# Performance work log

Hardware: AMD Instinct MI355X
Metric: run time of the kernel (lower is better)

The kernel has to match this reference:

```python
import jax, jax.numpy as jnp
import numpy as np
from jax import lax

B = 128
IM = 56  # im_size: 56 -> 48 -> 20 -> 6 spatial, 256*6*6/8 = 1152 primary capsules


def _conv(x, w, b, stride):
    y = lax.conv_general_dilated(x, w, (stride, stride), 'VALID',
                                 dimension_numbers=('NCHW', 'OIHW', 'NCHW'))
    return y + b[None, :, None, None]


def _squash(t, eps=1e-8):
    sn = jnp.sum(t * t, axis=-1, keepdims=True)
    return (sn / (1.0 + sn)) * t / jnp.sqrt(sn + eps)


def setup_inputs() -> dict:
    key = jax.random.key(0)
    ks = jax.random.split(key, 9)
    s = 0.02
    f32 = jnp.float32
    return {
        'x': jax.random.normal(ks[0], (B, 1, IM, IM), f32),
        'conv1_w': jax.random.normal(ks[1], (256, 1, 9, 9), f32) * s,
        'conv1_b': jnp.zeros((256,), f32),
        'conv2_w': jax.random.normal(ks[2], (256, 256, 9, 9), f32) * s,
        'conv2_b': jnp.zeros((256,), f32),
        'prim_w': jax.random.normal(ks[3], (256, 256, 9, 9), f32) * s,
        'prim_b': jnp.zeros((256,), f32),
        'W_digit': jax.random.normal(ks[4], (10, 1152, 8, 16), f32) * s,  # Linear(9216,16) per digit, reshaped
        'b_digit': jnp.zeros((10, 16), f32),
        'rec_w1': jax.random.normal(ks[5], (160, 512), f32) * s,
        'rec_b1': jnp.zeros((512,), f32),
        'rec_w2': jax.random.normal(ks[6], (512, 1024), f32) * s,
        'rec_b2': jnp.zeros((1024,), f32),
        'rec_w3': jax.random.normal(ks[7], (1024, IM * IM), f32) * s,
        'rec_b3': jnp.zeros((IM * IM,), f32),
    }


def reference(x, conv1_w, conv1_b, conv2_w, conv2_b, prim_w, prim_b,
              W_digit, b_digit, rec_w1, rec_b1, rec_w2, rec_b2, rec_w3, rec_b3):
    out = jax.nn.relu(_conv(x, conv1_w, conv1_b, 1))    # [B,256,48,48]
    out = jax.nn.relu(_conv(out, conv2_w, conv2_b, 2))  # [B,256,20,20]
    out = jax.nn.relu(_conv(out, prim_w, prim_b, 2))    # [B,256,6,6]
    u = _squash(out.reshape(out.shape[0], -1, 8))       # [B,1152,8]
    # fused 10-way digit-capsule transform: u_hat[b,i,j,:] = W[j,i] @ u[b,i]
    u_hat = jnp.einsum('bid,jido->bijo', u, W_digit)    # [B,1152,10,16]
    b_ij = jnp.zeros(u_hat.shape[:3], u_hat.dtype)      # [B,1152,10]
    num_iterations = 3
    v = None
    for it in range(num_iterations):
        c = jax.nn.softmax(b_ij, axis=1)                       # coupling over input capsules
        s_j = jnp.einsum('bij,bijo->bjo', c, u_hat) + b_digit  # [B,10,16]
        v = _squash(s_j)
        if it < num_iterations - 1:
            b_ij = b_ij + jnp.einsum('bijo,bjo->bij', u_hat, v)
    rec = v.reshape(v.shape[0], -1)                     # [B,160]
    rec = jax.nn.relu(rec @ rec_w1 + rec_b1)
    rec = jax.nn.relu(rec @ rec_w2 + rec_b2)
    rec = jax.nn.sigmoid(rec @ rec_w3 + rec_b3)         # [B,3136]
    return (v, rec)
```

## Files before the change

kernel.cpp:

```cpp
#include <hip/hip_runtime.h>
#include <hip/hip_bf16.h>

typedef float f32x4 __attribute__((ext_vector_type(4)));
typedef __bf16 bf16x8 __attribute__((ext_vector_type(8)));
typedef __bf16 bf16x4 __attribute__((ext_vector_type(4)));

#define AS1 __attribute__((address_space(1)))
#define AS3 __attribute__((address_space(3)))

__device__ __forceinline__ void gload16(const void* g, void* l) {
    __builtin_amdgcn_global_load_lds((AS1 unsigned int*)g, (AS3 unsigned int*)l, 16, 0, 0);
}

__device__ __forceinline__ float bfu(unsigned short u) {
    return __uint_as_float((unsigned)u << 16);
}

__global__ __launch_bounds__(256) void prep_w_kernel(const float* __restrict__ wA,
                                                     const float* __restrict__ wB,
                                                     __hip_bfloat16* __restrict__ wpA,
                                                     __hip_bfloat16* __restrict__ wpB,
                                                     const float* __restrict__ c1w,
                                                     __hip_bfloat16* __restrict__ wb,
                                                     const float* __restrict__ x,
                                                     __hip_bfloat16* __restrict__ xb) {
    int bid = blockIdx.x;
    int t = threadIdx.x;
    if (bid == 1024) {
        float tmp[81];
#pragma unroll
        for (int k = 0; k < 81; ++k) tmp[k] = c1w[t * 81 + k];
#pragma unroll
        for (int ks = 0; ks < 9; ++ks)
#pragma unroll
            for (int e = 0; e < 8; ++e)
                wb[(ks * 256 + t) * 8 + e] = __float2bfloat16(tmp[ks * 9 + e]);
#pragma unroll
        for (int e = 0; e < 8; ++e)
            wb[(9 * 256 + t) * 8 + e] = __float2bfloat16(tmp[e * 9 + 8]);
        wb[(10 * 256 + t) * 8 + 0] = __float2bfloat16(tmp[80]);
#pragma unroll
        for (int e = 1; e < 8; ++e) wb[(10 * 256 + t) * 8 + e] = __float2bfloat16(0.f);
#pragma unroll
        for (int e = 0; e < 8; ++e) wb[(11 * 256 + t) * 8 + e] = __float2bfloat16(0.f);
        return;
    }
    if (bid >= 1025) {
        long i4 = (long)(bid - 1025) * 1024 + t * 4;
        float4 v = *(const float4*)(x + i4);
        bf16x4 o = {(__bf16)v.x, (__bf16)v.y, (__bf16)v.z, (__bf16)v.w};
        *(bf16x4*)((__bf16*)xb + i4) = o;
        return;
    }
    __shared__ float wl[4 * 32 * 81];
    const float* w = (bid < 512) ? wA : wB;
    __hip_bfloat16* wp = (bid < 512) ? wpA : wpB;
    bid &= 511;
    int icg = bid & 7;
    int oc4 = (bid >> 3) & 31;
    int nblk = bid >> 8;
    int ocg0 = nblk * 128 + oc4 * 4;
    int ic0 = icg * 32;
    for (int f = t; f < 4 * 2592; f += 256) {
        int o = f / 2592;
        int rest = f - o * 2592;
        wl[f] = w[(ocg0 + o) * 20736 + ic0 * 81 + rest];
    }
    __syncthreads();
    for (int idx = t; idx < 81 * 128; idx += 256) {
        int kyx = idx >> 7;
        int o = (idx >> 5) & 3;
        int i = idx & 31;
        long dst = (long)(((kyx * 8 + icg) * 2 + nblk) * 128 + (oc4 * 4 + o)) * 32 + i;
        wp[dst] = __float2bfloat16(wl[o * 2592 + i * 81 + kyx]);
    }
}

__global__ __launch_bounds__(256) void conv1_mfma_kernel(const __hip_bfloat16* __restrict__ xb,
                                                         const __hip_bfloat16* __restrict__ wb,
                                                         const float* __restrict__ bias,
                                                         __hip_bfloat16* __restrict__ out) {
    __shared__ __bf16 Asl[640];
    int bid = blockIdx.x;
    int b = bid / 24, mb2 = bid - b * 24;
    int oy0 = mb2 * 2;
    int t = threadIdx.x;
    int lane = t & 63, wc = t >> 6;
    int q = lane >> 4;

    const __bf16* src = (const __bf16*)xb + b * 3136 + oy0 * 56;
    for (int idx = t; idx < 640; idx += 256) {
        int iy = idx >> 6, col = idx & 63;
        Asl[idx] = (col < 56) ? src[iy * 56 + col] : (__bf16)0.f;
    }

    bf16x8 Bf[3][4];
#pragma unroll
    for (int s = 0; s < 3; ++s)
#pragma unroll
        for (int ni = 0; ni < 4; ++ni) {
            int col = wc * 64 + ni * 16 + (lane & 15);
            Bf[s][ni] = *(const bf16x8*)(wb + ((s * 4 + q) * 256 + col) * 8);
        }

    f32x4 acc[6][4];
#pragma unroll
    for (int i = 0; i < 6; ++i)
#pragma unroll
        for (int j = 0; j < 4; ++j) acc[i][j] = (f32x4){0.f, 0.f, 0.f, 0.f};

    __syncthreads();

#pragma unroll
    for (int s = 0; s < 3; ++s) {
        int ks = s * 4 + q;
        bf16x8 af[6];
#pragma unroll
        for (int mi = 0; mi < 6; ++mi) {
            int r = mi * 16 + (lane & 15);
            int oyl = (r >= 48) ? 1 : 0;
            int ox = r - 48 * oyl;
            bf16x8 v;
            if (ks < 9) {
                __builtin_memcpy(&v, &Asl[(oyl + ks) * 64 + ox], 16);
            } else if (ks == 9) {
#pragma unroll
                for (int e = 0; e < 8; ++e) v[e] = Asl[(oyl + e) * 64 + ox + 8];
            } else if (ks == 10) {
#pragma unroll
                for (int e = 0; e < 8; ++e) v[e] = (__bf16)0.f;
                v[0] = Asl[(oyl + 8) * 64 + ox + 8];
            } else {
#pragma unroll
                for (int e = 0; e < 8; ++e) v[e] = (__bf16)0.f;
            }
            af[mi] = v;
        }
#pragma unroll
        for (int mi = 0; mi < 6; ++mi)
#pragma unroll
            for (int ni = 0; ni < 4; ++ni)
                acc[mi][ni] = __builtin_amdgcn_mfma_f32_16x16x32_bf16(af[mi], Bf[s][ni], acc[mi][ni], 0, 0, 0);
    }

    long m0 = (long)b * 2304 + mb2 * 96;
#pragma unroll
    for (int mi = 0; mi < 6; ++mi)
#pragma unroll
        for (int ni = 0; ni < 4; ++ni) {
            int col = wc * 64 + ni * 16 + (lane & 15);
            float bs = bias[col];
#pragma unroll
            for (int r2 = 0; r2 < 4; ++r2) {
                int row = mi * 16 + q * 4 + r2;
                float vv = acc[mi][ni][r2] + bs;
                vv = vv > 0.f ? vv : 0.f;
                out[(m0 + row) * 256 + col] = __float2bfloat16(vv);
            }
        }
}

__global__ __launch_bounds__(512, 2) void conv2_img_kernel(const __hip_bfloat16* __restrict__ in,
                                                           const __hip_bfloat16* __restrict__ wp,
                                                           const float* __restrict__ bias,
                                                           __hip_bfloat16* __restrict__ out) {
    __shared__ __hip_bfloat16 Ald[75264];
    int bid = blockIdx.x;
    int wg = (bid & 7) * 32 + (bid >> 3);
    int b = wg >> 1, nblk = wg & 1;
    int t = threadIdx.x;
    int lane = t & 63, wid = t >> 6;
    int wr = wid >> 1, wc = wid & 1;
    int ch8 = lane >> 4;

    const __hip_bfloat16* imgbase = in + (long)b * (48 * 48 * 256);
    const __hip_bfloat16* wpn = wp + (long)nblk * 4096 + (wc * 64 + (lane & 15)) * 32 + ch8 * 8;

    int qbase[7];
#pragma unroll
    for (int mi = 0; mi < 7; ++mi) {
        int ml = wr * 96 + mi * 16 + (lane & 15);
        int oy = ml / 20, ox = ml - oy * 20;
        qbase[mi] = ((2 * oy) * 49 + 2 * ox) * 4 + ch8;
    }

    f32x4 acc[7][4];
#pragma unroll
    for (int i = 0; i < 7; ++i)
#pragma unroll
        for (int j = 0; j < 4; ++j) acc[i][j] = (f32x4){0.f, 0.f, 0.f, 0.f};

    auto stageA = [&](int icg) {
#pragma unroll
        for (int c = 0; c < 3; ++c) {
            uint4 v[6];
#pragma unroll
            for (int j = 0; j < 6; ++j) {
                int gi = t + (c * 6 + j) * 512;
                int lrow = gi >> 2;
                int iy = lrow / 48;
                int col = lrow - iy * 48;
                if (iy > 46) iy = 46;
                v[j] = *(const uint4*)(imgbase + (iy * 48 + col) * 256 + icg * 32 + (gi & 3) * 8);
            }
#pragma unroll
            for (int j = 0; j < 6; ++j) {
                int gi = t + (c * 6 + j) * 512;
                int lrow = gi >> 2;
                int iy = lrow / 48;
                int col = lrow - iy * 48;
                int dst = (iy * 49 + col) * 4 + (gi & 3);
                int phys = dst ^ ((dst >> 3) & 7);
                *(uint4*)((char*)Ald + phys * 16) = v[j];
            }
        }
    };

    bf16x8 af_e[7], af_o[7], Be[4], Bo[4];
    int pf_kdelta = 0, pf_kx = 0, pf_ky = 0;
    auto prefA = [&](bf16x8* af) {
#pragma unroll
        for (int mi = 0; mi < 7; ++mi) {
            int qg = qbase[mi] + pf_kdelta;
            int phys = qg ^ ((qg >> 3) & 7);
            af[mi] = *(const bf16x8*)((const char*)Ald + phys * 16);
        }
        ++pf_kx; pf_kdelta += 4;
        if (pf_kx == 9) { pf_kx = 0; ++pf_ky; pf_kdelta = pf_ky * 196; }
    };
    auto domfma = [&](bf16x8* af, bf16x8* bf) {
        __builtin_amdgcn_s_setprio(1);
#pragma unroll
        for (int mi = 0; mi < 7; ++mi)
#pragma unroll
            for (int ni = 0; ni < 4; ++ni)
                acc[mi][ni] = __builtin_amdgcn_mfma_f32_16x16x32_bf16(af[mi], bf[ni], acc[mi][ni], 0, 0, 0);
        __builtin_amdgcn_s_setprio(0);
    };

    for (int icg = 0; icg < 8; ++icg) {
        const __hip_bfloat16* wpi = wpn + (long)icg * 8192;
        auto loadB = [&](bf16x8* dst, int kyx) {
            const __hip_bfloat16* p = wpi + (long)kyx * 65536;
#pragma unroll
            for (int ni = 0; ni < 4; ++ni) dst[ni] = *(const bf16x8*)(p + ni * 512);
        };
        if (icg) __builtin_amdgcn_s_barrier();
        loadB(Be, 0);
        loadB(Bo, 1);
        stageA(icg);
        asm volatile("s_waitcnt lgkmcnt(0)" ::: "memory");
        __builtin_amdgcn_s_barrier();
        if (wid >= 4) asm volatile("s_sleep 4");

        pf_kx = 0; pf_ky = 0; pf_kdelta = 0;
        prefA(af_e);
        for (int it2 = 0; it2 < 40; ++it2) {
            prefA(af_o);
            domfma(af_e, Be);
            loadB(Be, 2 * it2 + 2);
            prefA(af_e);
            domfma(af_o, Bo);
            loadB(Bo, 2 * it2 + 3);
        }
        domfma(af_e, Be);
    }

    int colbase = nblk * 128 + wc * 64 + (lane & 15);
#pragma unroll
    for (int mi = 0; mi < 7; ++mi) {
#pragma unroll
        for (int ni = 0; ni < 4; ++ni) {
            int col = colbase + ni * 16;
            float bs = bias[col];
#pragma unroll
            for (int r = 0; r < 4; ++r) {
                int ml = wr * 96 + mi * 16 + (lane >> 4) * 4 + r;
                float v = acc[mi][ni][r] + bs;
                v = v > 0.f ? v : 0.f;
                out[((long)b * 400 + ml) * 256 + col] = __float2bfloat16(v);
            }
        }
    }
}

__global__ __launch_bounds__(256) void conv_mfma_kernel(const __hip_bfloat16* __restrict__ in,
                                                        const __hip_bfloat16* __restrict__ wp,
                                                        const float* __restrict__ bias,
                                                        __hip_bfloat16* __restrict__ out,
                                                        __hip_bfloat16* __restrict__ part,
                                                        int Win, int imgStride, int HWout, int Wout,
                                                        int nkyx, int Mtot, int mode) {
    __shared__ __hip_bfloat16 Ald[3 * 4096];
    __shared__ __hip_bfloat16 Bld[3 * 4096];
    int mblk = blockIdx.x, nblk = blockIdx.y;
    int kyx0 = blockIdx.z * nkyx;
    int t = threadIdx.x;
    int lane = t & 63, wid = t >> 6;
    int swz = ((t & 3) ^ ((t >> 3) & 3)) * 8;
    int icsrc = swz;
    long bsrc = (t >> 2) * 32 + swz;

    long base0, base1;
    {
        int m = mblk * 128 + (t >> 2);
        int b = m / HWout; int rem = m - b * HWout;
        int oyy = rem / Wout; int oxx = rem - oyy * Wout;
        base0 = (long)b * imgStride + (long)(2 * oyy * Win + 2 * oxx) * 256;
        m += 64;
        b = m / HWout; rem = m - b * HWout;
        oyy = rem / Wout; oxx = rem - oyy * Wout;
        base1 = (long)b * imgStride + (long)(2 * oyy * Win + 2 * oxx) * 256;
    }

    f32x4 acc[4][4];
#pragma unroll
    for (int i = 0; i < 4; ++i)
#pragma unroll
        for (int j2 = 0; j2 < 4; ++j2) acc[i][j2] = (f32x4){0.f, 0.f, 0.f, 0.f};

    int wr = wid >> 1, wc = wid & 1;
    int slot8 = (((lane >> 4) ^ ((lane >> 1) & 3))) * 8;
    int a_off = ((wr * 64 + (lane & 15)) * 32 + slot8) * 2;
    int b_off = ((wc * 64 + (lane & 15)) * 32 + slot8) * 2;

    auto stage = [&](int s, int buf) {
        int kyx = kyx0 + (s >> 3);
        int icg = s & 7;
        int ky = kyx / 9, kx = kyx - ky * 9;
        long offA = (long)(ky * Win + kx) * 256 + icg * 32 + icsrc;
        long btb = (long)((kyx * 8 + icg) * 2 + nblk) * 4096 + bsrc;
        char* a0 = (char*)Ald + buf * 8192 + wid * 1024;
        char* b0 = (char*)Bld + buf * 8192 + wid * 1024;
        gload16(in + base0 + offA, a0);
        gload16(in + base1 + offA, a0 + 4096);
        gload16(wp + btb, b0);
        gload16(wp + btb + 2048, b0 + 4096);
    };

    int nsteps = nkyx * 8;
    stage(0, 0);
    stage(1, 1);
    stage(2, 2);
    int cur = 0;
    for (int s = 0; s < nsteps; ++s) {
        int rem = nsteps - 1 - s;
        if (rem >= 2) {
            asm volatile("s_waitcnt vmcnt(8)" ::: "memory");
        } else if (rem == 1) {
            asm volatile("s_waitcnt vmcnt(4)" ::: "memory");
        } else {
            asm volatile("s_waitcnt vmcnt(0)" ::: "memory");
        }
        __builtin_amdgcn_s_barrier();
        __builtin_amdgcn_sched_barrier(0);
        const char* Ac = (const char*)Ald + cur * 8192;
        const char* Bc = (const char*)Bld + cur * 8192;
        bf16x8 af[4], bfr[4];
#pragma unroll
        for (int i = 0; i < 4; ++i) af[i] = *(const bf16x8*)(Ac + a_off + i * 1024);
#pragma unroll
        for (int i = 0; i < 4; ++i) bfr[i] = *(const bf16x8*)(Bc + b_off + i * 1024);
#pragma unroll
        for (int mi = 0; mi < 4; ++mi)
#pragma unroll
            for (int ni = 0; ni < 4; ++ni)
                acc[mi][ni] = __builtin_amdgcn_mfma_f32_16x16x32_bf16(af[mi], bfr[ni], acc[mi][ni], 0, 0, 0);
        if (s + 3 < nsteps) {
            asm volatile("s_waitcnt lgkmcnt(0)" ::: "memory");
            __builtin_amdgcn_s_barrier();
            stage(s + 3, cur);
        }
        cur = (cur == 2) ? 0 : cur + 1;
    }

    int colbase = nblk * 128 + wc * 64 + (lane & 15);
    long mrowbase = (long)mblk * 128 + wr * 64 + (lane >> 4) * 4;
    if (mode == 0) {
#pragma unroll
        for (int mi = 0; mi < 4; ++mi) {
#pragma unroll
            for (int ni = 0; ni < 4; ++ni) {
                int col = colbase + ni * 16;
                float bs = bias[col];
#pragma unroll
                for (int r = 0; r < 4; ++r) {
                    long mrow = mrowbase + mi * 16 + r;
                    float v = acc[mi][ni][r] + bs;
                    v = v > 0.f ? v : 0.f;
                    out[mrow * 256 + col] = __float2bfloat16(v);
                }
            }
        }
    } else {
        __hip_bfloat16* pp = part + (long)blockIdx.z * Mtot * 256;
#pragma unroll
        for (int mi = 0; mi < 4; ++mi) {
#pragma unroll
            for (int ni = 0; ni < 4; ++ni) {
                int col = colbase + ni * 16;
#pragma unroll
                for (int r = 0; r < 4; ++r) {
                    long mrow = mrowbase + mi * 16 + r;
                    pp[mrow * 256 + col] = __float2bfloat16(acc[mi][ni][r]);
                }
            }
        }
    }
}

__global__ __launch_bounds__(256) void reduce_parts_kernel(const __hip_bfloat16* __restrict__ part,
                                                           const float* __restrict__ bias,
                                                           __hip_bfloat16* __restrict__ out) {
    int idx = blockIdx.x * 256 + threadIdx.x;
    float s = 0.f;
#pragma unroll
    for (int p = 0; p < 9; ++p) s += __bfloat162float(part[(long)p * 1179648 + idx]);
    s += bias[idx & 255];
    s = s > 0.f ? s : 0.f;
    out[idx] = __float2bfloat16(s);
}

__global__ __launch_bounds__(256) void squash_caps_kernel(const __hip_bfloat16* __restrict__ c3,
                                                          float* __restrict__ uT) {
    int g = blockIdx.x * 256 + threadIdx.x;
    int i = g >> 7, b = g & 127;
    float val[8];
    float sn = 0.f;
#pragma unroll
    for (int d = 0; d < 8; ++d) {
        int flat = i * 8 + d;
        int c = flat / 36; int rem = flat - c * 36;
        int y = rem / 6; int xx = rem - y * 6;
        float vv = __bfloat162float(c3[((b * 6 + y) * 6 + xx) * 256 + c]);
        val[d] = vv;
        sn += vv * vv;
    }
    float sc = (sn / (1.f + sn)) / sqrtf(sn + 1e-8f);
#pragma unroll
    for (int d = 0; d < 8; ++d) uT[(long)g * 8 + d] = val[d] * sc;
}

__global__ __launch_bounds__(256) void uhat_kernel(const float* __restrict__ uT,
                                                   const float* __restrict__ Wd,
                                                   __hip_bfloat16* __restrict__ uhat) {
    __shared__ float Wl2[1600];
    __shared__ float ul[1024];
    int i = blockIdx.x, t = threadIdx.x;
    for (int idx = t; idx < 1280; idx += 256) {
        int j = idx >> 7, rest = idx & 127;
        int d = rest >> 4, o = rest & 15;
        Wl2[(j * 16 + o) * 10 + d] = Wd[((long)j * 1152 + i) * 128 + rest];
    }
    {
        const float4* usrc = (const float4*)(uT + (long)i * 1024);
        float4* ud = (float4*)ul;
        ud[t] = usrc[t];
    }
    __syncthreads();
    int b = (t >= 160) ? 1 : 0;
    int jo = (t >= 160) ? t - 160 : t;
    for (int rr = 0; rr < 80; ++rr) {
        const float* up = &ul[b * 8];
        const float* wq = &Wl2[jo * 10];
        float a = 0.f;
#pragma unroll
        for (int d = 0; d < 8; ++d) a += up[d] * wq[d];
        int j = jo >> 4, o = jo & 15;
        uhat[(((long)b * 10 + j) * 1152 + i) * 16 + o] = __float2bfloat16(a);
        jo += 96; b += 1;
        if (jo >= 160) { jo -= 160; b += 1; }
    }
}

__global__ __launch_bounds__(256) void routing_kernel(const __hip_bfloat16* __restrict__ uhat,
                                                      const float* __restrict__ bdig,
                                                      float* __restrict__ vout,
                                                      float* __restrict__ vws) {
    __shared__ __hip_bfloat16 uh[1152 * 16];
    __shared__ float barr[1152];
    __shared__ float red[16];
    __shared__ float accb[16 * 256];
    __shared__ float svec[16];
    __shared__ float vsc[16];
    int bid = blockIdx.x;
    int j = bid % 10;
    int t = threadIdx.x;
    int wid = t >> 6;
    const uint4* srcp = (const uint4*)(uhat + (long)bid * 18432);
    uint4* dstp = (uint4*)uh;
    for (int idx = t; idx < 2304; idx += 256) dstp[idx] = srcp[idx];
    for (int idx = t; idx < 1152; idx += 256) barr[idx] = 0.f;
    __syncthreads();
    for (int it = 0; it < 3; ++it) {
        float lm = -1e30f;
        for (int i = t; i < 1152; i += 256) lm = fmaxf(lm, barr[i]);
#pragma unroll
        for (int m2 = 32; m2; m2 >>= 1) lm = fmaxf(lm, __shfl_xor(lm, m2));
        if ((t & 63) == 0) red[wid] = lm;
        __syncthreads();
        float mx = fmaxf(fmaxf(red[0], red[1]), fmaxf(red[2], red[3]));
        float le = 0.f;
        float a16[16];
#pragma unroll
        for (int o = 0; o < 16; ++o) a16[o] = 0.f;
        for (int i = t; i < 1152; i += 256) {
            float e = __expf(barr[i] - mx);
            le += e;
            const uint4* up = (const uint4*)(uh + i * 16);
            union { uint4 q; unsigned short s[8]; } U0, U1;
            U0.q = up[0]; U1.q = up[1];
#pragma unroll
            for (int o = 0; o < 8; ++o) a16[o] += e * bfu(U0.s[o]);
#pragma unroll
            for (int o = 0; o < 8; ++o) a16[8 + o] += e * bfu(U1.s[o]);
        }
#pragma unroll
        for (int m2 = 32; m2; m2 >>= 1) le += __shfl_xor(le, m2);
        if ((t & 63) == 0) red[4 + wid] = le;
#pragma unroll
        for (int o = 0; o < 16; ++o) accb[o * 256 + t] = a16[o];
        __syncthreads();
        float sume = red[4] + red[5] + red[6] + red[7];
        int g = t >> 4, tin = t & 15;
        float s = 0.f;
#pragma unroll
        for (int k = 0; k < 16; ++k) s += accb[g * 256 + tin + 16 * k];
#pragma unroll
        for (int m2 = 8; m2; m2 >>= 1) s += __shfl_xor(s, m2);
        if (tin == 0) svec[g] = s / sume + bdig[j * 16 + g];
        __syncthreads();
        if (t < 16) {
            float sv = svec[t];
            float sn = sv * sv;
#pragma unroll
            for (int m2 = 8; m2; m2 >>= 1) sn += __shfl_xor(sn, m2);
            float sc = (sn / (1.f + sn)) / sqrtf(sn + 1e-8f);
            float v = sv * sc;
            vsc[t] = v;
            if (it == 2) { vout[bid * 16 + t] = v; vws[bid * 16 + t] = v; }
        }
        __syncthreads();
        if (it < 2) {
            for (int i = t; i < 1152; i += 256) {
                const uint4* up = (const uint4*)(uh + i * 16);
                union { uint4 q; unsigned short s[8]; } U0, U1;
                U0.q = up[0]; U1.q = up[1];
                float dot = 0.f;
#pragma unroll
                for (int o = 0; o < 8; ++o) dot += vsc[o] * bfu(U0.s[o]);
#pragma unroll
                for (int o = 0; o < 8; ++o) dot += vsc[8 + o] * bfu(U1.s[o]);
                barr[i] += dot;
            }
            __syncthreads();
        }
    }
}

__global__ __launch_bounds__(256) void rec_gemm_kernel(const float* __restrict__ A,
                                                       const float* __restrict__ W,
                                                       const float* __restrict__ bias,
                                                       float* __restrict__ out,
                                                       int K, int N, int act) {
    __shared__ __align__(16) float As[2][2048];
    int n0 = blockIdx.x * 64;
    int bch = blockIdx.y * 32;
    int t = threadIdx.x;
    int n_l = t & 63, bh = t >> 6;
    const float* Wc = W + n0 + n_l;
    float acc[8];
#pragma unroll
    for (int i = 0; i < 8; ++i) acc[i] = 0.f;
    int T = (K + 63) >> 6;

    auto stageA = [&](int tile, int buf) {
        int k0 = tile << 6;
        for (int idx = t; idx < 2048; idx += 256) {
            int bb = idx >> 6, kk = idx & 63;
            As[buf][idx] = (k0 + kk < K) ? A[(long)(bch + bb) * K + k0 + kk] : 0.f;
        }
    };
    auto ldW = [&](int tile, float* w) {
        int k0 = tile << 6;
#pragma unroll
        for (int j = 0; j < 64; ++j) {
            int kr = k0 + j;
            if (kr >= K) kr = K - 1;
            w[j] = Wc[(long)kr * N];
        }
    };
    auto compute = [&](const float* w, int buf) {
#pragma unroll
        for (int bb = 0; bb < 8; ++bb) {
            const float4* ap = (const float4*)&As[buf][(bh * 8 + bb) * 64];
            float s = 0.f;
#pragma unroll
            for (int q = 0; q < 16; ++q) {
                float4 a = ap[q];
                s += a.x * w[q * 4] + a.y * w[q * 4 + 1] + a.z * w[q * 4 + 2] + a.w * w[q * 4 + 3];
            }
            acc[bb] += s;
        }
    };

    float wA[64], wB[64];
    ldW(0, wA);
    stageA(0, 0);
    __syncthreads();
    for (int tile = 0; tile < T; tile += 2) {
        if (tile + 1 < T) { ldW(tile + 1, wB); stageA(tile + 1, 1); }
        compute(wA, 0);
        __syncthreads();
        if (tile + 1 < T) {
            if (tile + 2 < T) { ldW(tile + 2, wA); stageA(tile + 2, 0); }
            compute(wB, 1);
            __syncthreads();
        }
    }

    float bs = bias[n0 + n_l];
#pragma unroll
    for (int bb = 0; bb < 8; ++bb) {
        float x = acc[bb] + bs;
        float r;
        if (act == 0) r = x > 0.f ? x : 0.f;
        else r = 1.f / (1.f + __expf(-x));
        out[(long)(bch + bh * 8 + bb) * N + n0 + n_l] = r;
    }
}

extern "C" void kernel_launch(void* const* d_in, const int* in_sizes, int n_in,
                              void* d_out, int out_size, void* d_ws, size_t ws_size,
                              hipStream_t stream) {
    const float* x   = (const float*)d_in[0];
    const float* c1w = (const float*)d_in[1];
    const float* c1b = (const float*)d_in[2];
    const float* c2w = (const float*)d_in[3];
    const float* c2b = (const float*)d_in[4];
    const float* pw  = (const float*)d_in[5];
    const float* pb  = (const float*)d_in[6];
    const float* Wd  = (const float*)d_in[7];
    const float* bd  = (const float*)d_in[8];
    const float* rw1 = (const float*)d_in[9];
    const float* rb1 = (const float*)d_in[10];
    const float* rw2 = (const float*)d_in[11];
    const float* rb2 = (const float*)d_in[12];
    const float* rw3 = (const float*)d_in[13];
    const float* rb3 = (const float*)d_in[14];
    float* outp = (float*)d_out;

    char* ws = (char*)d_ws;
    size_t off = 0;
    auto alloc = [&](size_t bytes) {
        char* p = ws + off;
        off += (bytes + 255) & ~(size_t)255;
        return p;
    };
    __hip_bfloat16* c1out = (__hip_bfloat16*)alloc(150994944UL);
    __hip_bfloat16* c2out = (__hip_bfloat16*)alloc(26214400UL);
    __hip_bfloat16* c3out = (__hip_bfloat16*)alloc(2359296UL);
    __hip_bfloat16* w2p   = (__hip_bfloat16*)alloc(10616832UL);
    __hip_bfloat16* w3p   = (__hip_bfloat16*)alloc(10616832UL);
    __hip_bfloat16* xb    = (__hip_bfloat16*)alloc(802816UL);
    __hip_bfloat16* wb    = (__hip_bfloat16*)alloc(49152UL);
    float* uT    = (float*)alloc(4718592UL);
    __hip_bfloat16* uhat = (__hip_bfloat16*)alloc(47185920UL);
    float* vws   = (float*)alloc(81920UL);
    float* rec1  = (float*)alloc(262144UL);
    float* rec2  = (float*)alloc(524288UL);

    __hip_bfloat16* c3part = (__hip_bfloat16*)uhat;

    prep_w_kernel<<<1417, 256, 0, stream>>>(c2w, pw, w2p, w3p, c1w, wb, x, xb);
    conv1_mfma_kernel<<<3072, 256, 0, stream>>>(xb, wb, c1b, c1out);
    conv2_img_kernel<<<256, 512, 0, stream>>>(c1out, w2p, c2b, c2out);
    conv_mfma_kernel<<<dim3(36, 2, 9), 256, 0, stream>>>(c2out, w3p, pb, c3out, c3part,
                                                         20, 20 * 20 * 256, 36, 6, 9, 4608, 1);
    reduce_parts_kernel<<<4608, 256, 0, stream>>>(c3part, pb, c3out);
    squash_caps_kernel<<<576, 256, 0, stream>>>(c3out, uT);
    uhat_kernel<<<1152, 256, 0, stream>>>(uT, Wd, uhat);
    routing_kernel<<<1280, 256, 0, stream>>>(uhat, bd, outp, vws);
    rec_gemm_kernel<<<dim3(8, 4), 256, 0, stream>>>(vws, rw1, rb1, rec1, 160, 512, 0);
    rec_gemm_kernel<<<dim3(16, 4), 256, 0, stream>>>(rec1, rw2, rb2, rec2, 512, 1024, 0);
    rec_gemm_kernel<<<dim3(49, 4), 256, 0, stream>>>(rec2, rw3, rb3, outp + 20480, 1024, 3136, 1);
}
```

Baseline: 807.1 us.

## Run conv2 in FP8 e4m3 with scaled MFMA and fp8 activations

Conv1 now writes its ReLU output as scaled FP8 e4m3 instead of bf16, and conv2 weights are quantized to scaled FP8 in a new layout during prep. Conv2 is rewritten to use the 16x16x128 f8f6f4 scaled MFMA, which processes four kernel taps per step, and the scale is undone in the epilogue. This halves conv1's output traffic and conv2's LDS and weight bandwidth while doubling MFMA throughput. In exchange it adds quantization error, and the custom e4m3 conversion truncates the mantissa and flushes subnormals to zero.

Measured after the change: 785.2 us. 2.7% less time.

```diff
diff --git a/kernel.cpp b/kernel.cpp
--- a/kernel.cpp
+++ b/kernel.cpp
@@ -4,6 +4,7 @@
 typedef float f32x4 __attribute__((ext_vector_type(4)));
 typedef __bf16 bf16x8 __attribute__((ext_vector_type(8)));
 typedef __bf16 bf16x4 __attribute__((ext_vector_type(4)));
+typedef int i32x8 __attribute__((ext_vector_type(8)));
 
 #define AS1 __attribute__((address_space(1)))
 #define AS3 __attribute__((address_space(3)))
@@ -16,17 +17,28 @@
     return __uint_as_float((unsigned)u << 16);
 }
 
-__global__ __launch_bounds__(256) void prep_w_kernel(const float* __restrict__ wA,
-                                                     const float* __restrict__ wB,
-                                                     __hip_bfloat16* __restrict__ wpA,
-                                                     __hip_bfloat16* __restrict__ wpB,
+__device__ __forceinline__ unsigned char f2e4m3s(float f) {
+    unsigned u = __float_as_uint(f);
+    unsigned s = (u >> 24) & 0x80;
+    unsigned ua = u & 0x7fffffffu;
+    int e = (int)(ua >> 23) - 127;
+    unsigned m = (ua >> 20) & 7;
+    if (e < -6) return (unsigned char)s;
+    if (e > 8 || (e == 8 && m > 6)) return (unsigned char)(s | 0x7e);
+    return (unsigned char)(s | ((unsigned)(e + 7) << 3) | m);
+}
+
+__global__ __launch_bounds__(256) void prep_w_kernel(const float* __restrict__ pw,
+                                                     __hip_bfloat16* __restrict__ w3p,
                                                      const float* __restrict__ c1w,
                                                      __hip_bfloat16* __restrict__ wb,
                                                      const float* __restrict__ x,
-                                                     __hip_bfloat16* __restrict__ xb) {
+                                                     __hip_bfloat16* __restrict__ xb,
+                                                     const float* __restrict__ c2w,
+                                                     unsigned char* __restrict__ wq2) {
     int bid = blockIdx.x;
     int t = threadIdx.x;
-    if (bid == 1024) {
+    if (bid == 512) {
         float tmp[81];
 #pragma unroll
         for (int k = 0; k < 81; ++k) tmp[k] = c1w[t * 81 + k];
@@ -45,17 +57,32 @@
         for (int e = 0; e < 8; ++e) wb[(11 * 256 + t) * 8 + e] = __float2bfloat16(0.f);
         return;
     }
-    if (bid >= 1025) {
-        long i4 = (long)(bid - 1025) * 1024 + t * 4;
+    if (bid >= 513 && bid < 905) {
+        long i4 = (long)(bid - 513) * 1024 + t * 4;
         float4 v = *(const float4*)(x + i4);
         bf16x4 o = {(__bf16)v.x, (__bf16)v.y, (__bf16)v.z, (__bf16)v.w};
         *(bf16x4*)((__bf16*)xb + i4) = o;
         return;
     }
+    if (bid >= 905) {
+        int b2 = bid - 905;
+        int icg = b2 / 42; int rem = b2 - icg * 42;
+        int ks = rem >> 1, nblk = rem & 1;
+        long base = (long)icg * 688128 + (long)ks * 32768 + (long)nblk * 16384;
+#pragma unroll
+        for (int u = 0; u < 64; ++u) {
+            int flat = t * 64 + u;
+            int ocl = flat >> 7, kb = flat & 127;
+            int kq = kb >> 5, icl = kb & 31;
+            int kyx = ks * 4 + kq;
+            float v = 0.f;
+            if (kyx < 81)
+                v = c2w[(long)(nblk * 128 + ocl) * 20736 + (icg * 32 + icl) * 81 + kyx] * 64.f;
+            wq2[base + flat] = f2e4m3s(v);
+        }
+        return;
+    }
     __shared__ float wl[4 * 32 * 81];
-    const float* w = (bid < 512) ? wA : wB;
-    __hip_bfloat16* wp = (bid < 512) ? wpA : wpB;
-    bid &= 511;
     int icg = bid & 7;
     int oc4 = (bid >> 3) & 31;
     int nblk = bid >> 8;
@@ -64,7 +91,7 @@
     for (int f = t; f < 4 * 2592; f += 256) {
         int o = f / 2592;
         int rest = f - o * 2592;
-        wl[f] = w[(ocg0 + o) * 20736 + ic0 * 81 + rest];
+        wl[f] = pw[(ocg0 + o) * 20736 + ic0 * 81 + rest];
     }
     __syncthreads();
     for (int idx = t; idx < 81 * 128; idx += 256) {
@@ -72,14 +99,14 @@
         int o = (idx >> 5) & 3;
         int i = idx & 31;
         long dst = (long)(((kyx * 8 + icg) * 2 + nblk) * 128 + (oc4 * 4 + o)) * 32 + i;
-        wp[dst] = __float2bfloat16(wl[o * 2592 + i * 81 + kyx]);
+        w3p[dst] = __float2bfloat16(wl[o * 2592 + i * 81 + kyx]);
     }
 }
 
 __global__ __launch_bounds__(256) void conv1_mfma_kernel(const __hip_bfloat16* __restrict__ xb,
                                                          const __hip_bfloat16* __restrict__ wb,
                                                          const float* __restrict__ bias,
-                                                         __hip_bfloat16* __restrict__ out) {
+                                                         unsigned char* __restrict__ out) {
     __shared__ __bf16 Asl[640];
     int bid = blockIdx.x;
     int b = bid / 24, mb2 = bid - b * 24;
@@ -155,33 +182,33 @@
                 int row = mi * 16 + q * 4 + r2;
                 float vv = acc[mi][ni][r2] + bs;
                 vv = vv > 0.f ? vv : 0.f;
-                out[(m0 + row) * 256 + col] = __float2bfloat16(vv);
+                out[(m0 + row) * 256 + col] = f2e4m3s(vv * 16.f);
             }
         }
 }
 
-__global__ __launch_bounds__(512, 2) void conv2_img_kernel(const __hip_bfloat16* __restrict__ in,
-                                                           const __hip_bfloat16* __restrict__ wp,
+__global__ __launch_bounds__(512, 2) void conv2_fp8_kernel(const unsigned char* __restrict__ in,
+                                                           const unsigned char* __restrict__ wq,
                                                            const float* __restrict__ bias,
                                                            __hip_bfloat16* __restrict__ out) {
-    __shared__ __hip_bfloat16 Ald[75264];
+    __shared__ unsigned char Ald[75264];
     int bid = blockIdx.x;
     int wg = (bid & 7) * 32 + (bid >> 3);
     int b = wg >> 1, nblk = wg & 1;
     int t = threadIdx.x;
     int lane = t & 63, wid = t >> 6;
     int wr = wid >> 1, wc = wid & 1;
-    int ch8 = lane >> 4;
-
-    const __hip_bfloat16* imgbase = in + (long)b * (48 * 48 * 256);
-    const __hip_bfloat16* wpn = wp + (long)nblk * 4096 + (wc * 64 + (lane & 15)) * 32 + ch8 * 8;
-
-    int qbase[7];
+    int kq = lane >> 4;
+
+    const unsigned char* imgbase = in + (long)b * (48 * 48 * 256);
+    const unsigned char* wqn = wq + ((long)(nblk * 128 + wc * 64 + (lane & 15))) * 128 + kq * 32;
+
+    int qrow[7];
 #pragma unroll
     for (int mi = 0; mi < 7; ++mi) {
         int ml = wr * 96 + mi * 16 + (lane & 15);
         int oy = ml / 20, ox = ml - oy * 20;
-        qbase[mi] = ((2 * oy) * 49 + 2 * ox) * 4 + ch8;
+        qrow[mi] = ((2 * oy) * 49 + 2 * ox) * 32;
     }
 
     f32x4 acc[7][4];
@@ -191,82 +218,67 @@
         for (int j = 0; j < 4; ++j) acc[i][j] = (f32x4){0.f, 0.f, 0.f, 0.f};
 
     auto stageA = [&](int icg) {
-#pragma unroll
-        for (int c = 0; c < 3; ++c) {
-            uint4 v[6];
-#pragma unroll
-            for (int j = 0; j < 6; ++j) {
-                int gi = t + (c * 6 + j) * 512;
-                int lrow = gi >> 2;
-                int iy = lrow / 48;
-                int col = lrow - iy * 48;
-                if (iy > 46) iy = 46;
-                v[j] = *(const uint4*)(imgbase + (iy * 48 + col) * 256 + icg * 32 + (gi & 3) * 8);
-            }
-#pragma unroll
-            for (int j = 0; j < 6; ++j) {
-                int gi = t + (c * 6 + j) * 512;
-                int lrow = gi >> 2;
-                int iy = lrow / 48;
-                int col = lrow - iy * 48;
-                int dst = (iy * 49 + col) * 4 + (gi & 3);
-                int phys = dst ^ ((dst >> 3) & 7);
-                *(uint4*)((char*)Ald + phys * 16) = v[j];
-            }
-        }
-    };
-
-    bf16x8 af_e[7], af_o[7], Be[4], Bo[4];
-    int pf_kdelta = 0, pf_kx = 0, pf_ky = 0;
-    auto prefA = [&](bf16x8* af) {
+#pragma unroll 3
+        for (int j = 0; j < 9; ++j) {
+            int gi = t + j * 512;
+            int row32 = gi >> 1, half = gi & 1;
+            int iy = row32 / 48, col = row32 - iy * 48;
+            uint4 v = *(const uint4*)(imgbase + ((long)(iy * 48 + col) * 256 + icg * 32 + half * 16));
+            *(uint4*)(Ald + (iy * 49 + col) * 32 + half * 16) = v;
+        }
+    };
+
+    union U8 { uint4 q[2]; i32x8 v; };
+    i32x8 Be[4], Bo[4];
+    auto loadB = [&](i32x8* dst, int icg, int ks) {
+        const unsigned char* p = wqn + (long)icg * 688128 + (long)ks * 32768;
+        uint4* d = (uint4*)dst;
+#pragma unroll
+        for (int ni = 0; ni < 4; ++ni) {
+            d[ni * 2]     = *(const uint4*)(p + ni * 2048);
+            d[ni * 2 + 1] = *(const uint4*)(p + ni * 2048 + 16);
+        }
+    };
+
+    auto step = [&](int icg, int ks, i32x8* Bcur, i32x8* Bnxt) {
+        if (ks + 1 < 21) loadB(Bnxt, icg, ks + 1);
+        int kyx = ks * 4 + kq;
+        int ky = kyx / 9;
+        int kdel = (kyx + 40 * ky) * 32;
+        __builtin_amdgcn_s_setprio(1);
 #pragma unroll
         for (int mi = 0; mi < 7; ++mi) {
-            int qg = qbase[mi] + pf_kdelta;
-            int phys = qg ^ ((qg >> 3) & 7);
-            af[mi] = *(const bf16x8*)((const char*)Ald + phys * 16);
-        }
-        ++pf_kx; pf_kdelta += 4;
-        if (pf_kx == 9) { pf_kx = 0; ++pf_ky; pf_kdelta = pf_ky * 196; }
-    };
-    auto domfma = [&](bf16x8* af, bf16x8* bf) {
-        __builtin_amdgcn_s_setprio(1);
-#pragma unroll
-        for (int mi = 0; mi < 7; ++mi)
+            const unsigned char* ap = Ald + qrow[mi] + kdel;
+            U8 a;
+            a.q[0] = *(const uint4*)ap;
+            a.q[1] = *(const uint4*)(ap + 16);
 #pragma unroll
             for (int ni = 0; ni < 4; ++ni)
-                acc[mi][ni] = __builtin_amdgcn_mfma_f32_16x16x32_bf16(af[mi], bf[ni], acc[mi][ni], 0, 0, 0);
+                acc[mi][ni] = __builtin_amdgcn_mfma_scale_f32_16x16x128_f8f6f4(
+                    a.v, Bcur[ni], acc[mi][ni],
+                    0, 0,
+                    0, 0x7F7F7F7F,
+                    0, 0x7F7F7F7F);
+        }
         __builtin_amdgcn_s_setprio(0);
     };
 
     for (int icg = 0; icg < 8; ++icg) {
-        const __hip_bfloat16* wpi = wpn + (long)icg * 8192;
-        auto loadB = [&](bf16x8* dst, int kyx) {
-            const __hip_bfloat16* p = wpi + (long)kyx * 65536;
-#pragma unroll
-            for (int ni = 0; ni < 4; ++ni) dst[ni] = *(const bf16x8*)(p + ni * 512);
-        };
         if (icg) __builtin_amdgcn_s_barrier();
-        loadB(Be, 0);
-        loadB(Bo, 1);
+        loadB(Be, icg, 0);
         stageA(icg);
         asm volatile("s_waitcnt lgkmcnt(0)" ::: "memory");
         __builtin_amdgcn_s_barrier();
         if (wid >= 4) asm volatile("s_sleep 4");
-
-        pf_kx = 0; pf_ky = 0; pf_kdelta = 0;
-        prefA(af_e);
-        for (int it2 = 0; it2 < 40; ++it2) {
-            prefA(af_o);
-            domfma(af_e, Be);
-            loadB(Be, 2 * it2 + 2);
-            prefA(af_e);
-            domfma(af_o, Bo);
-            loadB(Bo, 2 * it2 + 3);
-        }
-        domfma(af_e, Be);
+        for (int kk = 0; kk < 10; ++kk) {
+            step(icg, 2 * kk, Be, Bo);
+            step(icg, 2 * kk + 1, Bo, Be);
+        }
+        step(icg, 20, Be, Bo);
     }
 
     int colbase = nblk * 128 + wc * 64 + (lane & 15);
+    const float inv = 1.f / 1024.f;
 #pragma unroll
     for (int mi = 0; mi < 7; ++mi) {
 #pragma unroll
@@ -276,7 +288,7 @@
 #pragma unroll
             for (int r = 0; r < 4; ++r) {
                 int ml = wr * 96 + mi * 16 + (lane >> 4) * 4 + r;
-                float v = acc[mi][ni][r] + bs;
+                float v = acc[mi][ni][r] * inv + bs;
                 v = v > 0.f ? v : 0.f;
                 out[((long)b * 400 + ml) * 256 + col] = __float2bfloat16(v);
             }
@@ -657,11 +669,11 @@
         off += (bytes + 255) & ~(size_t)255;
         return p;
     };
-    __hip_bfloat16* c1out = (__hip_bfloat16*)alloc(150994944UL);
+    unsigned char* c1f8  = (unsigned char*)alloc(75497472UL);
     __hip_bfloat16* c2out = (__hip_bfloat16*)alloc(26214400UL);
     __hip_bfloat16* c3out = (__hip_bfloat16*)alloc(2359296UL);
-    __hip_bfloat16* w2p   = (__hip_bfloat16*)alloc(10616832UL);
     __hip_bfloat16* w3p   = (__hip_bfloat16*)alloc(10616832UL);
+    unsigned char* wq2    = (unsigned char*)alloc(5505024UL);
     __hip_bfloat16* xb    = (__hip_bfloat16*)alloc(802816UL);
     __hip_bfloat16* wb    = (__hip_bfloat16*)alloc(49152UL);
     float* uT    = (float*)alloc(4718592UL);
@@ -672,9 +684,9 @@
 
     __hip_bfloat16* c3part = (__hip_bfloat16*)uhat;
 
-    prep_w_kernel<<<1417, 256, 0, stream>>>(c2w, pw, w2p, w3p, c1w, wb, x, xb);
-    conv1_mfma_kernel<<<3072, 256, 0, stream>>>(xb, wb, c1b, c1out);
-    conv2_img_kernel<<<256, 512, 0, stream>>>(c1out, w2p, c2b, c2out);
+    prep_w_kernel<<<1241, 256, 0, stream>>>(pw, w3p, c1w, wb, x, xb, c2w, wq2);
+    conv1_mfma_kernel<<<3072, 256, 0, stream>>>(xb, wb, c1b, c1f8);
+    conv2_fp8_kernel<<<256, 512, 0, stream>>>(c1f8, wq2, c2b, c2out);
     conv_mfma_kernel<<<dim3(36, 2, 9), 256, 0, stream>>>(c2out, w3p, pb, c3out, c3part,
                                                          20, 20 * 20 * 256, 36, 6, 9, 4608, 1);
     reduce_parts_kernel<<<4608, 256, 0, stream>>>(c3part, pb, c3out);
```
